# Kernel optimization log

Measured on AMD Instinct MI355X. Metric: run time of the kernel, lower is better.

## Reference

```python
import jax, jax.numpy as jnp
import numpy as np

N_NODES = 20000
N_EDGES = 320000
D_IN = 128
D_OUT = 128
HEADS = 12
BN_EPS = 1e-5


def setup_inputs() -> dict:
    key = jax.random.key(0)
    ks = jax.random.split(key, 24)
    x = jax.random.normal(ks[0], (N_NODES, D_IN), dtype=jnp.float32)
    # edges guaranteed to have no self loops (so remove_self_loops is a no-op)
    src = jax.random.randint(ks[1], (N_EDGES,), 0, N_NODES, dtype=jnp.int32)
    off = jax.random.randint(ks[2], (N_EDGES,), 1, N_NODES, dtype=jnp.int32)
    dst = (src + off) % N_NODES
    edge_index = jnp.stack([src, dst], axis=0)
    inp = {"x": x, "edge_index": edge_index}
    # per-layer FeatureSteeredConvolution params (torch init: uniform weights, N(0,0.1) c/bias)
    dims_in = [D_IN, D_OUT, D_OUT]
    k = 3
    for li in range(3):
        din = dims_in[li]
        inp[f"l{li}_Wlin"] = jax.random.uniform(ks[k], (HEADS * D_OUT, din), dtype=jnp.float32); k += 1
        inp[f"l{li}_Wu"] = jax.random.uniform(ks[k], (HEADS, din), dtype=jnp.float32); k += 1
        inp[f"l{li}_c"] = 0.1 * jax.random.normal(ks[k], (HEADS,), dtype=jnp.float32); k += 1
        inp[f"l{li}_b"] = 0.1 * jax.random.normal(ks[k], (D_OUT,), dtype=jnp.float32); k += 1
    for bi in range(2):
        inp[f"bn{bi}_g"] = jnp.ones((D_OUT,), dtype=jnp.float32)
        inp[f"bn{bi}_b"] = jnp.zeros((D_OUT,), dtype=jnp.float32)
    return inp


def _fsc(x, src, dst, Wlin, Wu, c, b):
    """FeatureSteeredConvolution: edge gather -> softmax attention over heads ->
    per-head linear -> scatter-mean over destination nodes."""
    n = x.shape[0]
    x_j = x[src]                                  # [E, Cin] source features
    x_i = x[dst]                                  # [E, Cin] target features
    att = jax.nn.softmax((x_i - x_j) @ Wu.T + c, axis=1)   # [E, H]
    Wl = Wlin.reshape(HEADS, D_OUT, -1)           # [H, Cout, Cin]
    msg = jnp.zeros((src.shape[0], D_OUT), dtype=x.dtype)
    for h in range(HEADS):                        # small fixed loop over heads
        msg = msg + att[:, h:h + 1] * (x_j @ Wl[h].T)
    agg = jax.ops.segment_sum(msg, dst, num_segments=n)
    deg = jax.ops.segment_sum(jnp.ones((dst.shape[0],), dtype=x.dtype), dst, num_segments=n)
    return agg / jnp.maximum(deg, 1.0)[:, None] + b


def _bn(x, g, b):
    # BatchNorm1d in training mode: biased batch statistics
    m = jnp.mean(x, axis=0)
    v = jnp.var(x, axis=0)
    return (x - m) * jax.lax.rsqrt(v + BN_EPS) * g + b


def reference(x, edge_index, l0_Wlin, l0_Wu, l0_c, l0_b, bn0_g, bn0_b,
              l1_Wlin, l1_Wu, l1_c, l1_b, bn1_g, bn1_b,
              l2_Wlin, l2_Wu, l2_c, l2_b):
    n = x.shape[0]
    loops = jnp.arange(n, dtype=edge_index.dtype)
    src = jnp.concatenate([edge_index[0], loops])
    dst = jnp.concatenate([edge_index[1], loops])
    h = jax.nn.relu(_fsc(x, src, dst, l0_Wlin, l0_Wu, l0_c, l0_b))
    h = _bn(h, bn0_g, bn0_b)
    h = jax.nn.relu(_fsc(h, src, dst, l1_Wlin, l1_Wu, l1_c, l1_b))
    h = _bn(h, bn1_g, bn1_b)
    return _fsc(h, src, dst, l2_Wlin, l2_Wu, l2_c, l2_b)
```

## Files before the change

### kernel.cpp

```cpp
#include <hip/hip_runtime.h>
#include <hip/hip_bf16.h>

#define DHID 128
#define NH 12
#define KDIM 1536
#define KSPLIT 3
#define KSL (KDIM / KSPLIT)
#define COMBB 512

typedef __attribute__((ext_vector_type(8))) short short8;
typedef __attribute__((ext_vector_type(4))) float f32x4;

static __device__ __forceinline__ unsigned short f2bf(float f) {
  __hip_bfloat16 h = __float2bfloat16(f);
  return __builtin_bit_cast(unsigned short, h);
}
static __device__ __forceinline__ float bf2f(unsigned short u) {
  unsigned v = ((unsigned)u) << 16;
  return __builtin_bit_cast(float, v);
}


__global__ void hist_k(const int* __restrict__ dstp, int* __restrict__ cnt, int e0, int et) {
  int e = blockIdx.x * blockDim.x + threadIdx.x;
  if (e >= et) return;
  int d = (e < e0) ? dstp[e] : (e - e0);
  atomicAdd(&cnt[d], 1);
}

__global__ void scan_k(const int* __restrict__ cnt, int* __restrict__ row_start,
                       int* __restrict__ cursor, int n, int total) {
  __shared__ int part[1024];
  int t = threadIdx.x;
  const int CH = (n + 1023) >> 10;
  int base = t * CH;
  int s = 0;
  for (int j = 0; j < CH; ++j) { int i = base + j; if (i < n) s += cnt[i]; }
  part[t] = s;
  __syncthreads();
  for (int off = 1; off < 1024; off <<= 1) {
    int v = (t >= off) ? part[t - off] : 0;
    __syncthreads();
    part[t] += v;
    __syncthreads();
  }
  int run = (t == 0) ? 0 : part[t - 1];
  for (int j = 0; j < CH; ++j) {
    int i = base + j;
    if (i < n) {
      int c = cnt[i];
      row_start[i] = run;
      cursor[i] = run;
      run += c;
    }
  }
  if (t == 0) row_start[n] = total;
}

__global__ void scatter_k(const int* __restrict__ srcp, const int* __restrict__ dstp,
                          int* __restrict__ cursor, int* __restrict__ srcs,
                          int* __restrict__ dsts, int e0, int et) {
  int e = blockIdx.x * blockDim.x + threadIdx.x;
  if (e >= et) return;
  int s = (e < e0) ? srcp[e] : (e - e0);
  int d = (e < e0) ? dstp[e] : (e - e0);
  int pos = atomicAdd(&cursor[d], 1);
  srcs[pos] = s;
  dsts[pos] = d;
}


template<int BN>
__global__ void u_k(const float* __restrict__ in, const float* __restrict__ Wu,
                    const float* __restrict__ sc, const float* __restrict__ sh,
                    unsigned short* __restrict__ xb, float* __restrict__ u, int n) {
  int wid = (blockIdx.x * blockDim.x + threadIdx.x) >> 6;
  if (wid >= n) return;
  int lane = threadIdx.x & 63;
  float2 xv = *(const float2*)(in + (long)wid * DHID + 2 * lane);
  if (BN) {
    float2 scv = *(const float2*)(sc + 2 * lane);
    float2 shv = *(const float2*)(sh + 2 * lane);
    xv.x = xv.x * scv.x + shv.x;
    xv.y = xv.y * scv.y + shv.y;
  }
  unsigned pv = (unsigned)f2bf(xv.x) | ((unsigned)f2bf(xv.y) << 16);
  *(unsigned*)(xb + (long)wid * DHID + 2 * lane) = pv;
  #pragma unroll
  for (int h = 0; h < NH; ++h) {
    float2 wv = *(const float2*)(Wu + h * DHID + 2 * lane);
    float p = xv.x * wv.x + xv.y * wv.y;
    p += __shfl_xor(p, 1);  p += __shfl_xor(p, 2);  p += __shfl_xor(p, 4);
    p += __shfl_xor(p, 8);  p += __shfl_xor(p, 16); p += __shfl_xor(p, 32);
    if (lane == 0) u[wid * NH + h] = p;
  }
}


__global__ void att_k(const float* __restrict__ u, const float* __restrict__ cvec,
                      const int* __restrict__ srcs, const int* __restrict__ dsts,
                      const int* __restrict__ row_start, float* __restrict__ attS, int et) {
  int j = blockIdx.x * blockDim.x + threadIdx.x;
  if (j >= et) return;
  int s = srcs[j], d = dsts[j];
  const float4* ud = (const float4*)(u + (long)d * NH);
  const float4* us = (const float4*)(u + (long)s * NH);
  const float4* cp = (const float4*)cvec;
  float w[NH];
  #pragma unroll
  for (int q = 0; q < 3; ++q) {
    float4 a = ud[q], b = us[q], c = cp[q];
    w[4*q+0] = a.x - b.x + c.x;
    w[4*q+1] = a.y - b.y + c.y;
    w[4*q+2] = a.z - b.z + c.z;
    w[4*q+3] = a.w - b.w + c.w;
  }
  float m = w[0];
  #pragma unroll
  for (int h = 1; h < NH; ++h) m = fmaxf(m, w[h]);
  float ssum = 0.f;
  #pragma unroll
  for (int h = 0; h < NH; ++h) { w[h] = __expf(w[h] - m); ssum += w[h]; }
  float deg = (float)(row_start[d + 1] - row_start[d]);
  float inv = 1.f / (ssum * deg);
  float4* op = (float4*)(attS + (long)j * NH);
  #pragma unroll
  for (int q = 0; q < 3; ++q) {
    float4 v;
    v.x = w[4*q+0] * inv; v.y = w[4*q+1] * inv;
    v.z = w[4*q+2] * inv; v.w = w[4*q+3] * inv;
    op[q] = v;
  }
}


__global__ void edge_k(const unsigned short* __restrict__ xb, const float* __restrict__ attS,
                       const int* __restrict__ srcs, const int* __restrict__ row_start,
                       unsigned short* __restrict__ A, int n) {
  int wid = __builtin_amdgcn_readfirstlane((int)((blockIdx.x * blockDim.x + threadIdx.x) >> 6));
  if (wid >= n) return;
  int lane = threadIdx.x & 63;
  float acc[NH][2];
  #pragma unroll
  for (int h = 0; h < NH; ++h) { acc[h][0] = 0.f; acc[h][1] = 0.f; }
  int beg = row_start[wid], end = row_start[wid + 1];
  int j = beg;
  for (; j + 3 < end; j += 4) {
    int sx[4];
    #pragma unroll
    for (int i = 0; i < 4; ++i) sx[i] = srcs[j + i];
    unsigned pv[4];
    #pragma unroll
    for (int i = 0; i < 4; ++i)
      pv[i] = *(const unsigned*)(xb + (long)sx[i] * DHID + 2 * lane);
    const float4* ap = (const float4*)(attS + (long)j * NH);
    float4 aq[4][3];
    #pragma unroll
    for (int i = 0; i < 4; ++i) {
      aq[i][0] = ap[i * 3 + 0];
      aq[i][1] = ap[i * 3 + 1];
      aq[i][2] = ap[i * 3 + 2];
    }
    #pragma unroll
    for (int i = 0; i < 4; ++i) {
      float xv0 = bf2f((unsigned short)pv[i]);
      float xv1 = bf2f((unsigned short)(pv[i] >> 16));
      float av[NH];
      av[0]=aq[i][0].x; av[1]=aq[i][0].y; av[2] =aq[i][0].z; av[3] =aq[i][0].w;
      av[4]=aq[i][1].x; av[5]=aq[i][1].y; av[6] =aq[i][1].z; av[7] =aq[i][1].w;
      av[8]=aq[i][2].x; av[9]=aq[i][2].y; av[10]=aq[i][2].z; av[11]=aq[i][2].w;
      #pragma unroll
      for (int h = 0; h < NH; ++h) {
        acc[h][0] += av[h] * xv0;
        acc[h][1] += av[h] * xv1;
      }
    }
  }
  for (; j < end; ++j) {
    int s0 = srcs[j];
    unsigned pv = *(const unsigned*)(xb + (long)s0 * DHID + 2 * lane);
    float xv0 = bf2f((unsigned short)pv);
    float xv1 = bf2f((unsigned short)(pv >> 16));
    const float4* a0p = (const float4*)(attS + (long)j * NH);
    float4 a00 = a0p[0], a01 = a0p[1], a02 = a0p[2];
    float av0[NH];
    av0[0]=a00.x; av0[1]=a00.y; av0[2]=a00.z;  av0[3]=a00.w;
    av0[4]=a01.x; av0[5]=a01.y; av0[6]=a01.z;  av0[7]=a01.w;
    av0[8]=a02.x; av0[9]=a02.y; av0[10]=a02.z; av0[11]=a02.w;
    #pragma unroll
    for (int h = 0; h < NH; ++h) {
      acc[h][0] += av0[h] * xv0;
      acc[h][1] += av0[h] * xv1;
    }
  }
  unsigned* Ap = (unsigned*)(A + (long)wid * KDIM);
  #pragma unroll
  for (int h = 0; h < NH; ++h) {
    unsigned pv = (unsigned)f2bf(acc[h][0]) | ((unsigned)f2bf(acc[h][1]) << 16);
    Ap[h * (DHID / 2) + lane] = pv;
  }
}


__global__ void prep_wcat_k(const float* __restrict__ Wlin, unsigned short* __restrict__ Wcat) {
  int t = blockIdx.x * blockDim.x + threadIdx.x;
  int c = t / KDIM, f = t - c * KDIM;
  int h = f >> 7, k = f & (DHID - 1);
  Wcat[t] = f2bf(Wlin[((h << 7) + c) * DHID + k]);
}


__global__ __launch_bounds__(256) void gemm_k(
    const unsigned short* __restrict__ A, const unsigned short* __restrict__ B,
    float* __restrict__ part, float* __restrict__ outp, int M) {
  int w = threadIdx.x >> 6, lane = threadIdx.x & 63;
  int lr = lane & 15, lq = lane >> 4;
  int m0 = blockIdx.x * 64, n0 = w * 32;
  int ks = blockIdx.y;
  if (m0 >= M) return;
  f32x4 acc[4][2];
  #pragma unroll
  for (int mf = 0; mf < 4; ++mf)
    #pragma unroll
    for (int nf = 0; nf < 2; ++nf) acc[mf][nf] = (f32x4){0.f, 0.f, 0.f, 0.f};
  const short* Ap = (const short*)A;
  const short* Bp = (const short*)B;
  const long kbeg = (long)ks * KSL;
  long arow[4], brow[2];
  #pragma unroll
  for (int mf = 0; mf < 4; ++mf) arow[mf] = (long)(m0 + mf * 16 + lr) * KDIM + lq * 8 + kbeg;
  #pragma unroll
  for (int nf = 0; nf < 2; ++nf) brow[nf] = (long)(n0 + nf * 16 + lr) * KDIM + lq * 8 + kbeg;
  short8 ac[4], bc[2];
  #pragma unroll
  for (int mf = 0; mf < 4; ++mf) ac[mf] = *(const short8*)(Ap + arow[mf]);
  #pragma unroll
  for (int nf = 0; nf < 2; ++nf) bc[nf] = *(const short8*)(Bp + brow[nf]);
  #pragma unroll 2
  for (int kk = 0; kk < KSL; kk += 32) {
    const int kn = (kk + 32 < KSL) ? (kk + 32) : kk;
    short8 an[4], bn[2];
    #pragma unroll
    for (int mf = 0; mf < 4; ++mf) an[mf] = *(const short8*)(Ap + arow[mf] + kn);
    #pragma unroll
    for (int nf = 0; nf < 2; ++nf) bn[nf] = *(const short8*)(Bp + brow[nf] + kn);
    #pragma unroll
    for (int mf = 0; mf < 4; ++mf)
      #pragma unroll
      for (int nf = 0; nf < 2; ++nf)
        acc[mf][nf] = __builtin_amdgcn_mfma_f32_16x16x32_bf16(ac[mf], bc[nf], acc[mf][nf], 0, 0, 0);
    #pragma unroll
    for (int mf = 0; mf < 4; ++mf) ac[mf] = an[mf];
    #pragma unroll
    for (int nf = 0; nf < 2; ++nf) bc[nf] = bn[nf];
  }
  float* op = (ks == 0) ? outp : (part + (long)(ks - 1) * M * DHID);
  #pragma unroll
  for (int mf = 0; mf < 4; ++mf) {
    #pragma unroll
    for (int nf = 0; nf < 2; ++nf) {
      int c = n0 + nf * 16 + lr;
      int rowb = m0 + mf * 16 + lq * 4;
      #pragma unroll
      for (int r = 0; r < 4; ++r) {
        int row = rowb + r;
        if (row < M) op[(long)row * DHID + c] = acc[mf][nf][r];
      }
    }
  }
}


template<int RELU, int DOBN>
__global__ __launch_bounds__(256) void combine_k(
    const float* __restrict__ part, const float* __restrict__ bias,
    float* __restrict__ outp, float* __restrict__ bnpart, int M) {
  const int nvec = M * (DHID / 4);
  const int stride = COMBB * 256;
  int t0 = blockIdx.x * 256 + threadIdx.x;
  int c = (t0 & 31) * 4;
  float4 bc = *(const float4*)(bias + c);
  float s0=0,s1=0,s2=0,s3=0,q0=0,q1=0,q2=0,q3=0;
  for (int t = t0; t < nvec; t += stride) {
    long idx = (long)t * 4;
    float4 v  = *(const float4*)(outp + idx);
    float4 p1 = *(const float4*)(part + idx);
    float4 p2 = *(const float4*)(part + (long)M * DHID + idx);
    v.x += p1.x + p2.x + bc.x;
    v.y += p1.y + p2.y + bc.y;
    v.z += p1.z + p2.z + bc.z;
    v.w += p1.w + p2.w + bc.w;
    if (RELU) {
      v.x = fmaxf(v.x, 0.f); v.y = fmaxf(v.y, 0.f);
      v.z = fmaxf(v.z, 0.f); v.w = fmaxf(v.w, 0.f);
    }
    *(float4*)(outp + idx) = v;
    if (DOBN) {
      s0 += v.x; s1 += v.y; s2 += v.z; s3 += v.w;
      q0 += v.x*v.x; q1 += v.y*v.y; q2 += v.z*v.z; q3 += v.w*v.w;
    }
  }
  if (DOBN) {
    s0 += __shfl_xor(s0, 32); s1 += __shfl_xor(s1, 32);
    s2 += __shfl_xor(s2, 32); s3 += __shfl_xor(s3, 32);
    q0 += __shfl_xor(q0, 32); q1 += __shfl_xor(q1, 32);
    q2 += __shfl_xor(q2, 32); q3 += __shfl_xor(q3, 32);
    __shared__ float red[4][256];
    int w = threadIdx.x >> 6, lane = threadIdx.x & 63;
    if (lane < 32) {
      int cb = lane * 4;
      red[w][cb+0] = s0; red[w][cb+1] = s1; red[w][cb+2] = s2; red[w][cb+3] = s3;
      red[w][128+cb+0] = q0; red[w][128+cb+1] = q1; red[w][128+cb+2] = q2; red[w][128+cb+3] = q3;
    }
    __syncthreads();
    int tt = threadIdx.x;
    bnpart[blockIdx.x * 256 + tt] = red[0][tt] + red[1][tt] + red[2][tt] + red[3][tt];
  }
}


__global__ void bnfin_k(const float* __restrict__ bnpart,
                        const float* __restrict__ g, const float* __restrict__ b,
                        float* __restrict__ sc, float* __restrict__ sh, float invn) {
  __shared__ float col[256];
  int t = threadIdx.x;
  float s = 0.f;
  #pragma unroll 8
  for (int bb = 0; bb < COMBB; ++bb) s += bnpart[bb * 256 + t];
  col[t] = s;
  __syncthreads();
  if (t < DHID) {
    float m = col[t] * invn;
    float v = col[128 + t] * invn - m * m;
    float rs = rsqrtf(v + 1e-5f);
    float sg = g[t] * rs;
    sc[t] = sg;
    sh[t] = b[t] - m * sg;
  }
}


extern "C" void kernel_launch(void* const* d_in, const int* in_sizes, int n_in,
                              void* d_out, int out_size, void* d_ws, size_t ws_size,
                              hipStream_t stream) {
  const float* x = (const float*)d_in[0];
  const int* ei = (const int*)d_in[1];
  const int N = in_sizes[0] / DHID;
  const int E0 = in_sizes[1] / 2;
  const int ET = E0 + N;
  const int* srcp = ei;
  const int* dstp = ei + E0;
  const float* Wlin[3] = {(const float*)d_in[2], (const float*)d_in[6], (const float*)d_in[10]};
  const float* Wu[3]   = {(const float*)d_in[3], (const float*)d_in[7], (const float*)d_in[11]};
  const float* cc[3]   = {(const float*)d_in[4], (const float*)d_in[8], (const float*)d_in[12]};
  const float* bb[3]   = {(const float*)d_in[5], (const float*)d_in[9], (const float*)d_in[13]};
  const float* bng[2]  = {(const float*)d_in[14], (const float*)d_in[16]};
  const float* bnb[2]  = {(const float*)d_in[15], (const float*)d_in[17]};

  const int MPAD = ((N + 63) / 64) * 64;

  size_t o = 0;
  char* base = (char*)d_ws;
  auto carve = [&](size_t bytes) -> char* {
    char* p = base + o;
    o += (bytes + 255) & ~(size_t)255;
    return p;
  };
  int* row_start = (int*)carve((size_t)(N + 1) * 4);
  int* cursor    = (int*)carve((size_t)N * 4);
  int* srcs      = (int*)carve((size_t)ET * 4);
  int* dsts      = (int*)carve((size_t)ET * 4);
  float* u       = (float*)carve((size_t)N * NH * 4);
  float* bnpart  = (float*)carve((size_t)COMBB * 256 * 4);
  float* bnsc    = (float*)carve((size_t)DHID * 4);
  float* bnsh    = (float*)carve((size_t)DHID * 4);
  unsigned short* Wcat = (unsigned short*)carve((size_t)DHID * KDIM * 2);
  float* hA      = (float*)carve((size_t)N * DHID * 4);
  unsigned short* xb = (unsigned short*)carve((size_t)N * DHID * 2);
  unsigned short* A  = (unsigned short*)carve((size_t)MPAD * KDIM * 2);
  size_t attS_bytes = (size_t)ET * NH * 4;
  size_t part_bytes = (size_t)(KSPLIT - 1) * N * DHID * 4;
  char* shared_rg = carve(attS_bytes > part_bytes ? attS_bytes : part_bytes);
  float* attS = (float*)shared_rg;
  float* partb = (float*)shared_rg;
  (void)ws_size; (void)n_in; (void)out_size;

  const int EB = (ET + 255) / 256;
  const int NW = (N + 3) / 4;
  const int MB64 = (N + 63) / 64;

  hipMemsetAsync(cursor, 0, (size_t)N * 4, stream);
  hist_k<<<EB, 256, 0, stream>>>(dstp, cursor, E0, ET);
  scan_k<<<1, 1024, 0, stream>>>(cursor, row_start, cursor, N, ET);
  scatter_k<<<EB, 256, 0, stream>>>(srcp, dstp, cursor, srcs, dsts, E0, ET);

  for (int li = 0; li < 3; ++li) {
    const bool last = (li == 2);
    if (li == 0) u_k<0><<<NW, 256, 0, stream>>>(x, Wu[0], bnsc, bnsh, xb, u, N);
    else         u_k<1><<<NW, 256, 0, stream>>>(hA, Wu[li], bnsc, bnsh, xb, u, N);
    att_k<<<EB, 256, 0, stream>>>(u, cc[li], srcs, dsts, row_start, attS, ET);
    edge_k<<<NW, 256, 0, stream>>>(xb, attS, srcs, row_start, A, N);
    prep_wcat_k<<<(DHID * KDIM) / 256, 256, 0, stream>>>(Wlin[li], Wcat);
    float* outp = last ? (float*)d_out : hA;
    gemm_k<<<dim3(MB64, KSPLIT), 256, 0, stream>>>(A, Wcat, partb, outp, N);
    if (!last) {
      combine_k<1, 1><<<COMBB, 256, 0, stream>>>(partb, bb[li], outp, bnpart, N);
      bnfin_k<<<1, 256, 0, stream>>>(bnpart, bng[li], bnb[li], bnsc, bnsh, 1.f / (float)N);
    } else {
      combine_k<0, 0><<<COMBB, 256, 0, stream>>>(partb, bb[li], outp, bnpart, N);
    }
  }
}
```

Before: 542.1 us.

## Stage GEMM tiles through swizzled LDS with async double buffering; unroll edge loop by 8

The GEMM no longer has each wave load its A/B fragments straight from global memory. A 64-row A tile and the full 128-row B tile per 64-wide K chunk are now copied into LDS with global_load_lds, laid out with an XOR swizzle and double-buffered so the next chunk loads while the current one is computed. This lets the four waves share A loads instead of fetching them separately and aims to hide load latency. The edge aggregation loop is also unrolled from 4 to 8 edges, loading attention per edge inside the loop. The early return for out-of-range M is removed, so partial tiles depend on the padding of A.

```diff
diff --git a/kernel.cpp b/kernel.cpp
--- a/kernel.cpp
+++ b/kernel.cpp
@@ -6,6 +6,8 @@
 #define KDIM 1536
 #define KSPLIT 3
 #define KSL (KDIM / KSPLIT)
+#define BK 64
+#define NCHUNK (KSL / BK)
 #define COMBB 512
 
 typedef __attribute__((ext_vector_type(8))) short short8;
@@ -18,6 +20,11 @@
 static __device__ __forceinline__ float bf2f(unsigned short u) {
   unsigned v = ((unsigned)u) << 16;
   return __builtin_bit_cast(float, v);
+}
+static __device__ __forceinline__ void gload_lds16(const void* g, void* l) {
+  __builtin_amdgcn_global_load_lds(
+      (const __attribute__((address_space(1))) unsigned int*)g,
+      (__attribute__((address_space(3))) unsigned int*)l, 16, 0, 0);
 }
 
 
@@ -145,30 +152,24 @@
   for (int h = 0; h < NH; ++h) { acc[h][0] = 0.f; acc[h][1] = 0.f; }
   int beg = row_start[wid], end = row_start[wid + 1];
   int j = beg;
-  for (; j + 3 < end; j += 4) {
-    int sx[4];
-    #pragma unroll
-    for (int i = 0; i < 4; ++i) sx[i] = srcs[j + i];
-    unsigned pv[4];
-    #pragma unroll
-    for (int i = 0; i < 4; ++i)
+  for (; j + 7 < end; j += 8) {
+    int sx[8];
+    #pragma unroll
+    for (int i = 0; i < 8; ++i) sx[i] = srcs[j + i];
+    unsigned pv[8];
+    #pragma unroll
+    for (int i = 0; i < 8; ++i)
       pv[i] = *(const unsigned*)(xb + (long)sx[i] * DHID + 2 * lane);
-    const float4* ap = (const float4*)(attS + (long)j * NH);
-    float4 aq[4][3];
-    #pragma unroll
-    for (int i = 0; i < 4; ++i) {
-      aq[i][0] = ap[i * 3 + 0];
-      aq[i][1] = ap[i * 3 + 1];
-      aq[i][2] = ap[i * 3 + 2];
-    }
-    #pragma unroll
-    for (int i = 0; i < 4; ++i) {
+    #pragma unroll
+    for (int i = 0; i < 8; ++i) {
+      const float4* ap = (const float4*)(attS + (long)(j + i) * NH);
+      float4 a0 = ap[0], a1 = ap[1], a2 = ap[2];
       float xv0 = bf2f((unsigned short)pv[i]);
       float xv1 = bf2f((unsigned short)(pv[i] >> 16));
       float av[NH];
-      av[0]=aq[i][0].x; av[1]=aq[i][0].y; av[2] =aq[i][0].z; av[3] =aq[i][0].w;
-      av[4]=aq[i][1].x; av[5]=aq[i][1].y; av[6] =aq[i][1].z; av[7] =aq[i][1].w;
-      av[8]=aq[i][2].x; av[9]=aq[i][2].y; av[10]=aq[i][2].z; av[11]=aq[i][2].w;
+      av[0]=a0.x; av[1]=a0.y; av[2] =a0.z; av[3] =a0.w;
+      av[4]=a1.x; av[5]=a1.y; av[6] =a1.z; av[7] =a1.w;
+      av[8]=a2.x; av[9]=a2.y; av[10]=a2.z; av[11]=a2.w;
       #pragma unroll
       for (int h = 0; h < NH; ++h) {
         acc[h][0] += av[h] * xv0;
@@ -213,47 +214,79 @@
 __global__ __launch_bounds__(256) void gemm_k(
     const unsigned short* __restrict__ A, const unsigned short* __restrict__ B,
     float* __restrict__ part, float* __restrict__ outp, int M) {
+  __shared__ __align__(16) char smem[2 * 24576];
   int w = threadIdx.x >> 6, lane = threadIdx.x & 63;
   int lr = lane & 15, lq = lane >> 4;
   int m0 = blockIdx.x * 64, n0 = w * 32;
   int ks = blockIdx.y;
-  if (m0 >= M) return;
+  const long kbeg = (long)ks * KSL;
   f32x4 acc[4][2];
   #pragma unroll
   for (int mf = 0; mf < 4; ++mf)
     #pragma unroll
     for (int nf = 0; nf < 2; ++nf) acc[mf][nf] = (f32x4){0.f, 0.f, 0.f, 0.f};
-  const short* Ap = (const short*)A;
-  const short* Bp = (const short*)B;
-  const long kbeg = (long)ks * KSL;
-  long arow[4], brow[2];
-  #pragma unroll
-  for (int mf = 0; mf < 4; ++mf) arow[mf] = (long)(m0 + mf * 16 + lr) * KDIM + lq * 8 + kbeg;
-  #pragma unroll
-  for (int nf = 0; nf < 2; ++nf) brow[nf] = (long)(n0 + nf * 16 + lr) * KDIM + lq * 8 + kbeg;
-  short8 ac[4], bc[2];
-  #pragma unroll
-  for (int mf = 0; mf < 4; ++mf) ac[mf] = *(const short8*)(Ap + arow[mf]);
-  #pragma unroll
-  for (int nf = 0; nf < 2; ++nf) bc[nf] = *(const short8*)(Bp + brow[nf]);
-  #pragma unroll 2
-  for (int kk = 0; kk < KSL; kk += 32) {
-    const int kn = (kk + 32 < KSL) ? (kk + 32) : kk;
-    short8 an[4], bn[2];
-    #pragma unroll
-    for (int mf = 0; mf < 4; ++mf) an[mf] = *(const short8*)(Ap + arow[mf] + kn);
-    #pragma unroll
-    for (int nf = 0; nf < 2; ++nf) bn[nf] = *(const short8*)(Bp + brow[nf] + kn);
-    #pragma unroll
-    for (int mf = 0; mf < 4; ++mf)
+  const char* Ag = (const char*)A;
+  const char* Bg = (const char*)B;
+
+  auto stage = [&](int c, int p) {
+    const long kpos = kbeg + (long)c * BK;
+    #pragma unroll
+    for (int jj = 0; jj < 2; ++jj) {
+      int L = w * 2048 + jj * 1024 + lane * 16;
+      int r = L >> 7;
+      int srcin = (L & 127) ^ ((r & 7) << 4);
+      const char* g = Ag + ((long)(m0 + r) * KDIM + kpos) * 2 + srcin;
+      gload_lds16(g, &smem[p * 24576 + w * 2048 + jj * 1024]);
+    }
+    #pragma unroll
+    for (int jj = 0; jj < 4; ++jj) {
+      int L = w * 4096 + jj * 1024 + lane * 16;
+      int r = L >> 7;
+      int srcin = (L & 127) ^ ((r & 7) << 4);
+      const char* g = Bg + ((long)r * KDIM + kpos) * 2 + srcin;
+      gload_lds16(g, &smem[p * 24576 + 8192 + w * 4096 + jj * 1024]);
+    }
+  };
+
+  auto compute = [&](int p) {
+    const char* Ab = &smem[p * 24576];
+    const char* Bb = &smem[p * 24576 + 8192];
+    #pragma unroll
+    for (int kst = 0; kst < 2; ++kst) {
+      short8 av[4], bv[2];
       #pragma unroll
-      for (int nf = 0; nf < 2; ++nf)
-        acc[mf][nf] = __builtin_amdgcn_mfma_f32_16x16x32_bf16(ac[mf], bc[nf], acc[mf][nf], 0, 0, 0);
-    #pragma unroll
-    for (int mf = 0; mf < 4; ++mf) ac[mf] = an[mf];
-    #pragma unroll
-    for (int nf = 0; nf < 2; ++nf) bc[nf] = bn[nf];
-  }
+      for (int mf = 0; mf < 4; ++mf) {
+        int row = mf * 16 + lr;
+        int off = row * 128 + ((kst * 64 + lq * 16) ^ ((row & 7) << 4));
+        av[mf] = *(const short8*)(Ab + off);
+      }
+      #pragma unroll
+      for (int nf = 0; nf < 2; ++nf) {
+        int row = n0 + nf * 16 + lr;
+        int off = row * 128 + ((kst * 64 + lq * 16) ^ ((row & 7) << 4));
+        bv[nf] = *(const short8*)(Bb + off);
+      }
+      #pragma unroll
+      for (int mf = 0; mf < 4; ++mf)
+        #pragma unroll
+        for (int nf = 0; nf < 2; ++nf)
+          acc[mf][nf] = __builtin_amdgcn_mfma_f32_16x16x32_bf16(av[mf], bv[nf], acc[mf][nf], 0, 0, 0);
+    }
+  };
+
+  stage(0, 0);
+  for (int c = 0; c < NCHUNK; ++c) {
+    if (c + 1 < NCHUNK) {
+      stage(c + 1, (c + 1) & 1);
+      asm volatile("s_waitcnt vmcnt(6)" ::: "memory");
+    } else {
+      asm volatile("s_waitcnt vmcnt(0)" ::: "memory");
+    }
+    __syncthreads();
+    compute(c & 1);
+    __syncthreads();
+  }
+
   float* op = (ks == 0) ? outp : (part + (long)(ks - 1) * M * DHID);
   #pragma unroll
   for (int mf = 0; mf < 4; ++mf) {
```

New measurement: 461.9 us. 1.17x faster.
